# Performance work log

Hardware: AMD Instinct MI355X
Metric: run time of the kernel (lower is better)

Reference implementation:

```python
import jax, jax.numpy as jnp
import numpy as np

B, T, D = 4, 8192, 1024
C = 8.0


def setup_inputs() -> dict:
    key = jax.random.key(0)
    k1, k2, k3 = jax.random.split(key, 3)
    init_std = D ** (-0.5)
    x = jax.random.normal(k1, (B, T, D), dtype=jnp.float32)
    W_in = jax.random.truncated_normal(k2, -3.0, 3.0, (D, D), dtype=jnp.float32) * init_std
    W_gate = jax.random.truncated_normal(k3, -3.0, 3.0, (D, D), dtype=jnp.float32) * init_std
    b_in = jnp.zeros((D,), dtype=jnp.float32)
    b_gate = jnp.zeros((D,), dtype=jnp.float32)
    forget_lambda = jnp.linspace(-4.323, -9.0, D, dtype=jnp.float32)
    return {"x": x, "W_in": W_in, "b_in": b_in, "W_gate": W_gate,
            "b_gate": b_gate, "forget_lambda": forget_lambda}


def _combine(c1, c2):
    # linear recurrence h_t = a_t * h_{t-1} + b_t  (associative composition)
    a1, b1 = c1
    a2, b2 = c2
    return a1 * a2, a2 * b1 + b2


def reference(x, W_in, b_in, W_gate, b_gate, forget_lambda):
    # x: [B, T, D]
    input_gate = x @ W_in.T + b_in          # [B, T, D]
    recurrence_gate = x @ W_gate.T + b_gate  # [B, T, D]
    alpha = jnp.exp(-C * jax.nn.softplus(forget_lambda) * jax.nn.sigmoid(recurrence_gate))
    beta = jnp.sqrt(1.0 - alpha ** 2 + 1e-6)
    xbeta = beta * jax.nn.sigmoid(input_gate) * x
    # parallel scan of h_t = alpha_t * h_{t-1} + xbeta_t along sequence axis
    _, h = jax.lax.associative_scan(_combine, (alpha, xbeta), axis=1)
    return h
```

## Files before the change

kernel.cpp:

```cpp
#include <hip/hip_runtime.h>

typedef unsigned short u16;
typedef __attribute__((ext_vector_type(8))) short short8;
typedef __attribute__((ext_vector_type(4))) float f32x4;

#define T_SEQ 8192
#define DDIM 1024
#define BB 4
#define MM (BB * T_SEQ)
#define NC 128
#define CHUNK (T_SEQ / NC)
#define CHAINS (BB * DDIM)

__device__ __forceinline__ float bf_lo(unsigned p) {
    union { unsigned u; float f; } v; v.u = p << 16; return v.f;
}
__device__ __forceinline__ float bf_hi(unsigned p) {
    union { unsigned u; float f; } v; v.u = p & 0xffff0000u; return v.f;
}
__device__ __forceinline__ float bf_u16(u16 p) {
    union { unsigned u; float f; } v; v.u = ((unsigned)p) << 16; return v.f;
}
__device__ __forceinline__ u16 f2bf(float f) {
    union { unsigned u; float f; } v; v.f = f;
    unsigned r = v.u + 0x7fffu + ((v.u >> 16) & 1u);
    return (u16)(r >> 16);
}
__device__ __forceinline__ float sigm(float z) {
    return __builtin_amdgcn_rcpf(1.0f + __expf(-z));
}
__device__ __forceinline__ void gld16(const u16* g, u16* l) {
    __builtin_amdgcn_global_load_lds((const __attribute__((address_space(1))) void*)g,
                                     (__attribute__((address_space(3))) void*)l, 16, 0, 0);
}

#define N4X (MM * DDIM / 4)
#define N4W (DDIM * DDIM / 4)
__global__ __launch_bounds__(256) void cvt_all(const float* __restrict__ x,
                                               const float* __restrict__ Wi,
                                               const float* __restrict__ Wg,
                                               u16* __restrict__ Xb,
                                               u16* __restrict__ Wib,
                                               u16* __restrict__ Wgb) {
    int i = blockIdx.x * 256 + threadIdx.x;
    const float* src; u16* dst; int j;
    if (i < N4X)            { src = x;  dst = Xb;  j = i; }
    else if (i < N4X + N4W) { src = Wi; dst = Wib; j = i - N4X; }
    else                    { src = Wg; dst = Wgb; j = i - N4X - N4W; }
    float4 v = ((const float4*)src)[j];
    ushort4 o;
    o.x = f2bf(v.x); o.y = f2bf(v.y); o.z = f2bf(v.z); o.w = f2bf(v.w);
    ((ushort4*)dst)[j] = o;
}


#define MROW(i_, av)                                                                   \
    acc[i_][0] = __builtin_amdgcn_mfma_f32_16x16x32_bf16(av, b0, acc[i_][0], 0, 0, 0); \
    acc[i_][1] = __builtin_amdgcn_mfma_f32_16x16x32_bf16(av, b1, acc[i_][1], 0, 0, 0); \
    acc[i_][2] = __builtin_amdgcn_mfma_f32_16x16x32_bf16(av, b2, acc[i_][2], 0, 0, 0); \
    acc[i_][3] = __builtin_amdgcn_mfma_f32_16x16x32_bf16(av, b3, acc[i_][3], 0, 0, 0);

#define LDA_S(s_, i) (*(const short8*)&lds[(s_)*8192 + (arow0 + (i)*16)*32 + aoff])
#define LDB_S(s_, j) (*(const short8*)&lds[32768 + (s_)*8192 + (brow0 + (j)*16)*32 + aoff])

#define STA_S(ds_, ht_, rb) gld16(gA + (size_t)(ht_)*32 + (size_t)(rb)*128*DDIM,       \
                                  &lds[(ds_)*8192 + (rb)*4096 + tid*8])
#define STB_S(ds_, ht_, hf) gld16(((hf) ? gBg : gBi) + (size_t)(ht_)*32,               \
                                  &lds[32768 + (ds_)*8192 + (hf)*4096 + tid*8])

#define PHASE_A(s_, ds_, ht_, DOST)                                                    \
    b0 = LDB_S(s_, 0); b1 = LDB_S(s_, 1); b2 = LDB_S(s_, 2); b3 = LDB_S(s_, 3);        \
    a0 = LDA_S(s_, 0); a1 = LDA_S(s_, 1); a2 = LDA_S(s_, 2); a3 = LDA_S(s_, 3);        \
    if (DOST) { STA_S(ds_, ht_, 0); STA_S(ds_, ht_, 1); }                              \
    __builtin_amdgcn_s_barrier();                                                      \
    asm volatile("s_waitcnt lgkmcnt(0)" ::: "memory");                                 \
    __builtin_amdgcn_sched_barrier(0);                                                 \
    __builtin_amdgcn_s_setprio(1);                                                     \
    MROW(0, a0) MROW(1, a1) MROW(2, a2) MROW(3, a3)                                    \
    __builtin_amdgcn_s_setprio(0);                                                     \
    __builtin_amdgcn_s_barrier();

#define PHASE_B(s_, ds_, ht_, DOST, VMS)                                               \
    a0 = LDA_S(s_, 4); a1 = LDA_S(s_, 5); a2 = LDA_S(s_, 6); a3 = LDA_S(s_, 7);        \
    if (DOST) { STB_S(ds_, ht_, 0); STB_S(ds_, ht_, 1); }                              \
    asm volatile("s_waitcnt " VMS ::: "memory");                                       \
    __builtin_amdgcn_s_barrier();                                                      \
    asm volatile("s_waitcnt lgkmcnt(0)" ::: "memory");                                 \
    __builtin_amdgcn_sched_barrier(0);                                                 \
    __builtin_amdgcn_s_setprio(1);                                                     \
    MROW(4, a0) MROW(5, a1) MROW(6, a2) MROW(7, a3)                                    \
    __builtin_amdgcn_s_setprio(0);                                                     \
    __builtin_amdgcn_s_barrier();

#define PAIR(s_, ds_, ht_, DOST, VMS)                                                  \
    PHASE_A(s_, ds_, ht_, DOST)                                                        \
    PHASE_B(s_, ds_, ht_, DOST, VMS)

__global__ __launch_bounds__(512, 2)
void gemm_fused(const u16* __restrict__ X, const u16* __restrict__ Wi,
                const u16* __restrict__ Wg, const float* __restrict__ b_in,
                const float* __restrict__ b_gate, const float* __restrict__ lam,
                u16* __restrict__ Sg, u16* __restrict__ XBg,
                float* __restrict__ AggA, float* __restrict__ AggB) {
    const int bid = blockIdx.x;
    const int xcd = bid & 7;
    const int r = bid >> 3;
    const int n_tile = r & 7;
    const int m_tile = xcd * 16 + (r >> 3);
    const int tN0 = n_tile * 128;
    const int tM0 = m_tile * 256;

    const int tid = threadIdx.x;
    const int lane = tid & 63;
    const int w = tid >> 6;
    const int wm = w >> 2;
    const int wn = w & 3;
    const int gate = wn >> 1;
    const int wn_sub = wn & 1;

    __shared__ u16 lds[65536];

    const int srow = tid >> 2;
    const int c8log = (tid & 3) ^ ((tid >> 3) & 3);
    const u16* gA  = X  + (size_t)(tM0 + srow) * DDIM + c8log * 8;
    const u16* gBi = Wi + (size_t)(tN0 + srow) * DDIM + c8log * 8;
    const u16* gBg = Wg + (size_t)(tN0 + srow) * DDIM + c8log * 8;

    const int lm = lane & 15;
    const int aoff = (((lane >> 4) ^ ((lm >> 1) & 3))) * 8;
    const int arow0 = wm * 128 + lm;
    const int brow0 = gate * 128 + wn_sub * 64 + lm;

    f32x4 acc[8][4] = {};
    short8 a0, a1, a2, a3, b0, b1, b2, b3;

    STA_S(0, 0, 0); STA_S(0, 0, 1); STB_S(0, 0, 0); STB_S(0, 0, 1);
    STA_S(1, 1, 0); STA_S(1, 1, 1); STB_S(1, 1, 0); STB_S(1, 1, 1);
    STA_S(2, 2, 0); STA_S(2, 2, 1); STB_S(2, 2, 0); STB_S(2, 2, 1);
    asm volatile("s_waitcnt vmcnt(8)" ::: "memory");
    __builtin_amdgcn_s_barrier();

    for (int g = 0; g < 7; ++g) {
        const int hb = 4 * g;
        PAIR(0, 3, hb + 3, 1, "vmcnt(8)")
        PAIR(1, 0, hb + 4, 1, "vmcnt(8)")
        PAIR(2, 1, hb + 5, 1, "vmcnt(8)")
        PAIR(3, 2, hb + 6, 1, "vmcnt(8)")
    }
    PAIR(0, 3, 31, 1, "vmcnt(8)")
    PAIR(1, 0, 0, 0, "vmcnt(4)")
    PAIR(2, 0, 0, 0, "vmcnt(0)")
    PAIR(3, 0, 0, 0, "vmcnt(0)")

    const int r0 = (lane >> 4) << 2;
    const int cb = lane & 15;
    if (gate) {
#pragma unroll
        for (int j = 0; j < 4; ++j) {
            const int colg = tN0 + wn_sub * 64 + j * 16 + cb;
            const int cl = wn_sub * 64 + j * 16 + cb;
            const float bj = b_gate[colg];
            const float nsp = -8.0f * log1pf(__expf(lam[colg]));
#pragma unroll
            for (int i = 0; i < 8; ++i) {
                const int rl0 = wm * 128 + i * 16 + r0;
#pragma unroll
                for (int rr = 0; rr < 4; ++rr) {
                    const int rl = rl0 + rr;
                    float s = nsp * sigm(acc[i][j][rr] + bj);
                    lds[rl * 128 + (cl ^ (((rl >> 2) & 7) << 4))] = f2bf(s);
                }
            }
        }
    } else {
#pragma unroll
        for (int j = 0; j < 4; ++j) {
            const int colg = tN0 + wn_sub * 64 + j * 16 + cb;
            const int cl = wn_sub * 64 + j * 16 + cb;
            const float bj = b_in[colg];
#pragma unroll
            for (int i = 0; i < 8; ++i) {
                const int rl0 = wm * 128 + i * 16 + r0;
#pragma unroll
                for (int rr = 0; rr < 4; ++rr) {
                    const int rl = rl0 + rr;
                    float p = sigm(acc[i][j][rr] + bj);
                    lds[32768 + rl * 128 + (cl ^ (((rl >> 2) & 7) << 4))] =
                        (u16)(p * 65535.0f + 0.5f);
                }
            }
        }
    }
    asm volatile("s_waitcnt lgkmcnt(0)" ::: "memory");
    __builtin_amdgcn_s_barrier();
    __builtin_amdgcn_sched_barrier(0);

    const int cc = tid & 15;
    const int rg0 = (tid >> 4) * 8;
    float Aacc[8] = {1.f, 1.f, 1.f, 1.f, 1.f, 1.f, 1.f, 1.f};
    float Bacc[8] = {};
#pragma unroll
    for (int k = 0; k < 8; ++k) {
        const int rl = rg0 + k;
        const int ch = (cc ^ (((rl >> 2) & 7) << 1)) * 8;
        short8 sv = *(const short8*)&lds[rl * 128 + ch];
        short8 pv = *(const short8*)&lds[32768 + rl * 128 + ch];
        const size_t go = (size_t)(tM0 + rl) * DDIM + tN0 + cc * 8;
        short8 xv = *(const short8*)&X[go];
        short8 ov;
#pragma unroll
        for (int e = 0; e < 8; ++e) {
            float s = bf_u16((u16)sv[e]);
            float p = (float)((u16)pv[e]) * (1.0f / 65535.0f);
            float xf = bf_u16((u16)xv[e]);
            float be = sqrtf(1.0f - __expf(2.0f * s) + 1e-6f);
            u16 xbq = f2bf(be * p * xf);
            ov[e] = (short)xbq;
            float a = __expf(s);
            Bacc[e] = fmaf(a, Bacc[e], bf_u16(xbq));
            Aacc[e] *= a;
        }
        *(short8*)&Sg[go] = sv;
        *(short8*)&XBg[go] = ov;
    }

    asm volatile("s_waitcnt lgkmcnt(0)" ::: "memory");
    __builtin_amdgcn_s_barrier();
    {
        float* fA = (float*)lds;
        float* fB = (float*)lds + 4096;
        const int seg = tid >> 4;
#pragma unroll
        for (int e = 0; e < 8; ++e) {
            fA[seg * 128 + cc * 8 + e] = Aacc[e];
            fB[seg * 128 + cc * 8 + e] = Bacc[e];
        }
        asm volatile("s_waitcnt lgkmcnt(0)" ::: "memory");
        __builtin_amdgcn_s_barrier();
        const int chk = tid >> 7;
        const int col = tid & 127;
        float A = 1.0f, Bv = 0.0f;
#pragma unroll
        for (int k = 0; k < 8; ++k) {
            float a = fA[(chk * 8 + k) * 128 + col];
            float b = fB[(chk * 8 + k) * 128 + col];
            Bv = fmaf(a, Bv, b);
            A *= a;
        }
        const int bq = tM0 >> 13;
        const int cw = ((tM0 & 8191) >> 6) + chk;
        const size_t gi = (size_t)cw * CHAINS + bq * DDIM + tN0 + col;
        AggA[gi] = A;
        AggB[gi] = Bv;
    }
}

__global__ __launch_bounds__(256)
void scan_pass2(const float* __restrict__ AggA, const float* __restrict__ AggB,
                float* __restrict__ H0) {
    const int chain = blockIdx.x * 256 + threadIdx.x;
    float p = 0.0f;
#pragma unroll 8
    for (int c = 0; c < NC; c++) {
        H0[(size_t)c * CHAINS + chain] = p;
        p = AggA[(size_t)c * CHAINS + chain] * p + AggB[(size_t)c * CHAINS + chain];
    }
}

__global__ __launch_bounds__(256)
void scan_pass3(const u16* __restrict__ S, const u16* __restrict__ XB,
                const float* __restrict__ H0, float* __restrict__ out) {
    const int c = blockIdx.x, bq = blockIdx.z;
    const int d0 = threadIdx.x * 4;
    size_t base = ((size_t)(bq * T_SEQ + c * CHUNK)) * DDIM + d0;
    const int chain = bq * DDIM + d0;

    float4 h = *(const float4*)(H0 + (size_t)c * CHAINS + chain);
#pragma unroll 4
    for (int t = 0; t < CHUNK; t++) {
        ushort4 sp = *(const ushort4*)(S + base);
        ushort4 xp = *(const ushort4*)(XB + base);
        h.x = fmaf(__expf(bf_u16(sp.x)), h.x, bf_u16(xp.x));
        h.y = fmaf(__expf(bf_u16(sp.y)), h.y, bf_u16(xp.y));
        h.z = fmaf(__expf(bf_u16(sp.z)), h.z, bf_u16(xp.z));
        h.w = fmaf(__expf(bf_u16(sp.w)), h.w, bf_u16(xp.w));
        *(float4*)(out + base) = h;
        base += DDIM;
    }
}

extern "C" void kernel_launch(void* const* d_in, const int* in_sizes, int n_in,
                              void* d_out, int out_size, void* d_ws, size_t ws_size,
                              hipStream_t stream) {
    const float* x   = (const float*)d_in[0];
    const float* Win = (const float*)d_in[1];
    const float* bin = (const float*)d_in[2];
    const float* Wg  = (const float*)d_in[3];
    const float* bg  = (const float*)d_in[4];
    const float* lam = (const float*)d_in[5];
    float* out = (float*)d_out;

    char* w = (char*)d_ws;
    u16* Wi_bf  = (u16*)(w);
    u16* Wg_bf  = (u16*)(w + (size_t)(2) * 1024 * 1024);
    u16* Sg     = (u16*)(w + (size_t)(4) * 1024 * 1024);
    u16* XBg    = (u16*)(w + (size_t)(68) * 1024 * 1024);
    float* AggA = (float*)(w + (size_t)(132) * 1024 * 1024);
    float* AggB = (float*)(w + (size_t)(134) * 1024 * 1024);
    float* H0   = (float*)(w + (size_t)(136) * 1024 * 1024);

    u16* Xbf = (u16*)d_out;

    cvt_all<<<dim3((N4X + 2 * N4W) / 256), dim3(256), 0, stream>>>(
        x, Win, Wg, Xbf, Wi_bf, Wg_bf);

    gemm_fused<<<dim3((DDIM / 128) * (MM / 256)), dim3(512), 0, stream>>>(
        Xbf, Wi_bf, Wg_bf, bin, bg, lam, Sg, XBg, AggA, AggB);

    scan_pass2<<<dim3(CHAINS / 256), dim3(256), 0, stream>>>(AggA, AggB, H0);
    scan_pass3<<<dim3(NC, 1, BB), dim3(256), 0, stream>>>(Sg, XBg, H0, out);
}
```

Baseline: 461.5 us.

## Shrink fused GEMM tile to 128 rows with 256-thread blocks and 3-stage pipeline

The fused GEMM block is cut from 256x256 (512 threads, 4 warp rows) to a 128-row M tile with 256 threads. Each warp now owns 64 rows and one full 128-column gate, so it holds 4x8 accumulators. The LDS ring drops from 4 stages to 3 and uses a smaller shared buffer, with the global-to-LDS loads re-split across the two MFMA phases. This doubles the grid and cuts LDS use per block, which should improve occupancy and load balance. In exchange, each block gets less operand reuse and issues more global loads per FLOP.

```diff
diff --git a/kernel.cpp b/kernel.cpp
--- a/kernel.cpp
+++ b/kernel.cpp
@@ -54,49 +54,49 @@
 }
 
 
-#define MROW(i_, av)                                                                   \
-    acc[i_][0] = __builtin_amdgcn_mfma_f32_16x16x32_bf16(av, b0, acc[i_][0], 0, 0, 0); \
-    acc[i_][1] = __builtin_amdgcn_mfma_f32_16x16x32_bf16(av, b1, acc[i_][1], 0, 0, 0); \
-    acc[i_][2] = __builtin_amdgcn_mfma_f32_16x16x32_bf16(av, b2, acc[i_][2], 0, 0, 0); \
-    acc[i_][3] = __builtin_amdgcn_mfma_f32_16x16x32_bf16(av, b3, acc[i_][3], 0, 0, 0);
-
-#define LDA_S(s_, i) (*(const short8*)&lds[(s_)*8192 + (arow0 + (i)*16)*32 + aoff])
-#define LDB_S(s_, j) (*(const short8*)&lds[32768 + (s_)*8192 + (brow0 + (j)*16)*32 + aoff])
-
-#define STA_S(ds_, ht_, rb) gld16(gA + (size_t)(ht_)*32 + (size_t)(rb)*128*DDIM,       \
-                                  &lds[(ds_)*8192 + (rb)*4096 + tid*8])
-#define STB_S(ds_, ht_, hf) gld16(((hf) ? gBg : gBi) + (size_t)(ht_)*32,               \
-                                  &lds[32768 + (ds_)*8192 + (hf)*4096 + tid*8])
-
-#define PHASE_A(s_, ds_, ht_, DOST)                                                    \
-    b0 = LDB_S(s_, 0); b1 = LDB_S(s_, 1); b2 = LDB_S(s_, 2); b3 = LDB_S(s_, 3);        \
-    a0 = LDA_S(s_, 0); a1 = LDA_S(s_, 1); a2 = LDA_S(s_, 2); a3 = LDA_S(s_, 3);        \
-    if (DOST) { STA_S(ds_, ht_, 0); STA_S(ds_, ht_, 1); }                              \
-    __builtin_amdgcn_s_barrier();                                                      \
-    asm volatile("s_waitcnt lgkmcnt(0)" ::: "memory");                                 \
-    __builtin_amdgcn_sched_barrier(0);                                                 \
-    __builtin_amdgcn_s_setprio(1);                                                     \
-    MROW(0, a0) MROW(1, a1) MROW(2, a2) MROW(3, a3)                                    \
-    __builtin_amdgcn_s_setprio(0);                                                     \
+#define MROWJ(i_, av, J)                                                                     \
+    acc[i_][(J)+0] = __builtin_amdgcn_mfma_f32_16x16x32_bf16(av, b0, acc[i_][(J)+0], 0,0,0); \
+    acc[i_][(J)+1] = __builtin_amdgcn_mfma_f32_16x16x32_bf16(av, b1, acc[i_][(J)+1], 0,0,0); \
+    acc[i_][(J)+2] = __builtin_amdgcn_mfma_f32_16x16x32_bf16(av, b2, acc[i_][(J)+2], 0,0,0); \
+    acc[i_][(J)+3] = __builtin_amdgcn_mfma_f32_16x16x32_bf16(av, b3, acc[i_][(J)+3], 0,0,0);
+
+#define MQUADJ(J) MROWJ(0, a0, J) MROWJ(1, a1, J) MROWJ(2, a2, J) MROWJ(3, a3, J)
+
+#define LDA_S(s_, i) (*(const short8*)&lds[(s_)*4096 + (arow0 + (i)*16)*32 + aoff])
+#define LDB_S(s_, j) (*(const short8*)&lds[12288 + (s_)*8192 + (brow0 + (j)*16)*32 + aoff])
+
+#define STA_R(s_, ht_, rb) gld16(gA + (size_t)(ht_)*32 + (size_t)(rb)*64*DDIM,               \
+                                 &lds[(s_)*4096 + (rb)*2048 + tid*8])
+#define STB_R(s_, ht_, rb) gld16(((rb) < 2 ? gBi + (size_t)(rb)*64*DDIM                      \
+                                           : gBg + (size_t)((rb)-2)*64*DDIM)                 \
+                                     + (size_t)(ht_)*32,                                     \
+                                 &lds[12288 + (s_)*8192 + (rb)*2048 + tid*8])
+
+#define PAIRX(s_, ss_, ht_, DOST, VMS)                                                       \
+                                                                           \
+    b0 = LDB_S(s_, 0); b1 = LDB_S(s_, 1); b2 = LDB_S(s_, 2); b3 = LDB_S(s_, 3);              \
+    a0 = LDA_S(s_, 0); a1 = LDA_S(s_, 1); a2 = LDA_S(s_, 2); a3 = LDA_S(s_, 3);              \
+    if (DOST) { STA_R(ss_, ht_, 0); STA_R(ss_, ht_, 1); STB_R(ss_, ht_, 0); }                \
+    __builtin_amdgcn_s_barrier();                                                            \
+    asm volatile("s_waitcnt lgkmcnt(0)" ::: "memory");                                       \
+    __builtin_amdgcn_sched_barrier(0);                                                       \
+    __builtin_amdgcn_s_setprio(1);                                                           \
+    MQUADJ(0)                                                                                \
+    __builtin_amdgcn_s_setprio(0);                                                           \
+    __builtin_amdgcn_s_barrier();                                                            \
+                                                                           \
+    b0 = LDB_S(s_, 4); b1 = LDB_S(s_, 5); b2 = LDB_S(s_, 6); b3 = LDB_S(s_, 7);              \
+    if (DOST) { STB_R(ss_, ht_, 1); STB_R(ss_, ht_, 2); STB_R(ss_, ht_, 3); }                \
+    asm volatile("s_waitcnt " VMS ::: "memory");                                             \
+    __builtin_amdgcn_s_barrier();                                                            \
+    asm volatile("s_waitcnt lgkmcnt(0)" ::: "memory");                                       \
+    __builtin_amdgcn_sched_barrier(0);                                                       \
+    __builtin_amdgcn_s_setprio(1);                                                           \
+    MQUADJ(4)                                                                                \
+    __builtin_amdgcn_s_setprio(0);                                                           \
     __builtin_amdgcn_s_barrier();
 
-#define PHASE_B(s_, ds_, ht_, DOST, VMS)                                               \
-    a0 = LDA_S(s_, 4); a1 = LDA_S(s_, 5); a2 = LDA_S(s_, 6); a3 = LDA_S(s_, 7);        \
-    if (DOST) { STB_S(ds_, ht_, 0); STB_S(ds_, ht_, 1); }                              \
-    asm volatile("s_waitcnt " VMS ::: "memory");                                       \
-    __builtin_amdgcn_s_barrier();                                                      \
-    asm volatile("s_waitcnt lgkmcnt(0)" ::: "memory");                                 \
-    __builtin_amdgcn_sched_barrier(0);                                                 \
-    __builtin_amdgcn_s_setprio(1);                                                     \
-    MROW(4, a0) MROW(5, a1) MROW(6, a2) MROW(7, a3)                                    \
-    __builtin_amdgcn_s_setprio(0);                                                     \
-    __builtin_amdgcn_s_barrier();
-
-#define PAIR(s_, ds_, ht_, DOST, VMS)                                                  \
-    PHASE_A(s_, ds_, ht_, DOST)                                                        \
-    PHASE_B(s_, ds_, ht_, DOST, VMS)
-
-__global__ __launch_bounds__(512, 2)
+__global__ __launch_bounds__(256, 2)
 void gemm_fused(const u16* __restrict__ X, const u16* __restrict__ Wi,
                 const u16* __restrict__ Wg, const float* __restrict__ b_in,
                 const float* __restrict__ b_gate, const float* __restrict__ lam,
@@ -106,19 +106,17 @@
     const int xcd = bid & 7;
     const int r = bid >> 3;
     const int n_tile = r & 7;
-    const int m_tile = xcd * 16 + (r >> 3);
+    const int m_tile = xcd * 32 + (r >> 3);
     const int tN0 = n_tile * 128;
-    const int tM0 = m_tile * 256;
+    const int tM0 = m_tile * 128;
 
     const int tid = threadIdx.x;
     const int lane = tid & 63;
     const int w = tid >> 6;
-    const int wm = w >> 2;
-    const int wn = w & 3;
-    const int gate = wn >> 1;
-    const int wn_sub = wn & 1;
-
-    __shared__ u16 lds[65536];
+    const int wm = w & 1;
+    const int gate = w >> 1;
+
+    __shared__ u16 lds[36864];
 
     const int srow = tid >> 2;
     const int c8log = (tid & 3) ^ ((tid >> 3) & 3);
@@ -128,42 +126,38 @@
 
     const int lm = lane & 15;
     const int aoff = (((lane >> 4) ^ ((lm >> 1) & 3))) * 8;
-    const int arow0 = wm * 128 + lm;
-    const int brow0 = gate * 128 + wn_sub * 64 + lm;
-
-    f32x4 acc[8][4] = {};
+    const int arow0 = wm * 64 + lm;
+    const int brow0 = gate * 128 + lm;
+
+    f32x4 acc[4][8] = {};
     short8 a0, a1, a2, a3, b0, b1, b2, b3;
 
-    STA_S(0, 0, 0); STA_S(0, 0, 1); STB_S(0, 0, 0); STB_S(0, 0, 1);
-    STA_S(1, 1, 0); STA_S(1, 1, 1); STB_S(1, 1, 0); STB_S(1, 1, 1);
-    STA_S(2, 2, 0); STA_S(2, 2, 1); STB_S(2, 2, 0); STB_S(2, 2, 1);
-    asm volatile("s_waitcnt vmcnt(8)" ::: "memory");
+    STA_R(0, 0, 0); STA_R(0, 0, 1); STB_R(0, 0, 0); STB_R(0, 0, 1); STB_R(0, 0, 2); STB_R(0, 0, 3);
+    STA_R(1, 1, 0); STA_R(1, 1, 1); STB_R(1, 1, 0); STB_R(1, 1, 1); STB_R(1, 1, 2); STB_R(1, 1, 3);
+    asm volatile("s_waitcnt vmcnt(6)" ::: "memory");
     __builtin_amdgcn_s_barrier();
 
-    for (int g = 0; g < 7; ++g) {
-        const int hb = 4 * g;
-        PAIR(0, 3, hb + 3, 1, "vmcnt(8)")
-        PAIR(1, 0, hb + 4, 1, "vmcnt(8)")
-        PAIR(2, 1, hb + 5, 1, "vmcnt(8)")
-        PAIR(3, 2, hb + 6, 1, "vmcnt(8)")
-    }
-    PAIR(0, 3, 31, 1, "vmcnt(8)")
-    PAIR(1, 0, 0, 0, "vmcnt(4)")
-    PAIR(2, 0, 0, 0, "vmcnt(0)")
-    PAIR(3, 0, 0, 0, "vmcnt(0)")
+    for (int g = 0; g < 10; ++g) {
+        const int hb = 3 * g;
+        PAIRX(0, 2, hb + 2, 1, "vmcnt(6)")
+        PAIRX(1, 0, hb + 3, 1, "vmcnt(6)")
+        PAIRX(2, 1, hb + 4, 1, "vmcnt(6)")
+    }
+    PAIRX(0, 0, 0, 0, "vmcnt(0)")
+    PAIRX(1, 0, 0, 0, "vmcnt(0)")
 
     const int r0 = (lane >> 4) << 2;
     const int cb = lane & 15;
     if (gate) {
 #pragma unroll
-        for (int j = 0; j < 4; ++j) {
-            const int colg = tN0 + wn_sub * 64 + j * 16 + cb;
-            const int cl = wn_sub * 64 + j * 16 + cb;
+        for (int j = 0; j < 8; ++j) {
+            const int colg = tN0 + j * 16 + cb;
+            const int cl = j * 16 + cb;
             const float bj = b_gate[colg];
             const float nsp = -8.0f * log1pf(__expf(lam[colg]));
 #pragma unroll
-            for (int i = 0; i < 8; ++i) {
-                const int rl0 = wm * 128 + i * 16 + r0;
+            for (int i = 0; i < 4; ++i) {
+                const int rl0 = wm * 64 + i * 16 + r0;
 #pragma unroll
                 for (int rr = 0; rr < 4; ++rr) {
                     const int rl = rl0 + rr;
@@ -174,18 +168,18 @@
         }
     } else {
 #pragma unroll
-        for (int j = 0; j < 4; ++j) {
-            const int colg = tN0 + wn_sub * 64 + j * 16 + cb;
-            const int cl = wn_sub * 64 + j * 16 + cb;
+        for (int j = 0; j < 8; ++j) {
+            const int colg = tN0 + j * 16 + cb;
+            const int cl = j * 16 + cb;
             const float bj = b_in[colg];
 #pragma unroll
-            for (int i = 0; i < 8; ++i) {
-                const int rl0 = wm * 128 + i * 16 + r0;
+            for (int i = 0; i < 4; ++i) {
+                const int rl0 = wm * 64 + i * 16 + r0;
 #pragma unroll
                 for (int rr = 0; rr < 4; ++rr) {
                     const int rl = rl0 + rr;
                     float p = sigm(acc[i][j][rr] + bj);
-                    lds[32768 + rl * 128 + (cl ^ (((rl >> 2) & 7) << 4))] =
+                    lds[16384 + rl * 128 + (cl ^ (((rl >> 2) & 7) << 4))] =
                         (u16)(p * 65535.0f + 0.5f);
                 }
             }
@@ -204,7 +198,7 @@
         const int rl = rg0 + k;
         const int ch = (cc ^ (((rl >> 2) & 7) << 1)) * 8;
         short8 sv = *(const short8*)&lds[rl * 128 + ch];
-        short8 pv = *(const short8*)&lds[32768 + rl * 128 + ch];
+        short8 pv = *(const short8*)&lds[16384 + rl * 128 + ch];
         const size_t go = (size_t)(tM0 + rl) * DDIM + tN0 + cc * 8;
         short8 xv = *(const short8*)&X[go];
         short8 ov;
@@ -228,7 +222,7 @@
     __builtin_amdgcn_s_barrier();
     {
         float* fA = (float*)lds;
-        float* fB = (float*)lds + 4096;
+        float* fB = (float*)lds + 2048;
         const int seg = tid >> 4;
 #pragma unroll
         for (int e = 0; e < 8; ++e) {
@@ -314,7 +308,7 @@
     cvt_all<<<dim3((N4X + 2 * N4W) / 256), dim3(256), 0, stream>>>(
         x, Win, Wg, Xbf, Wi_bf, Wg_bf);
 
-    gemm_fused<<<dim3((DDIM / 128) * (MM / 256)), dim3(512), 0, stream>>>(
+    gemm_fused<<<dim3((DDIM / 128) * (MM / 128)), dim3(256), 0, stream>>>(
         Xbf, Wi_bf, Wg_bf, bin, bg, lam, Sg, XBg, AggA, AggB);
 
     scan_pass2<<<dim3(CHAINS / 256), dim3(256), 0, stream>>>(AggA, AggB, H0);
```

After: 452.0 us. -2.1%, faster.
